# Performance work log

Measured on AMD Instinct MI355X. Metric: run time of the kernel, lower is better.

## Reference

```python
import jax, jax.numpy as jnp
import numpy as np

B, T, C = 4, 4096, 1024


def setup_inputs() -> dict:
    key = jax.random.key(0)
    ks = jax.random.split(key, 5)
    s = 1.0 / np.sqrt(C)
    x = jax.random.normal(ks[0], (B, T, C), dtype=jnp.float32)
    Wq = jax.random.normal(ks[1], (C, C), dtype=jnp.float32) * s
    Wk = jax.random.normal(ks[2], (C, C), dtype=jnp.float32) * s
    Wv = jax.random.normal(ks[3], (C, C), dtype=jnp.float32) * s
    Wo = jax.random.normal(ks[4], (C, C), dtype=jnp.float32) * s
    bo = jnp.zeros((C,), dtype=jnp.float32)
    return {"x": x, "Wq": Wq, "Wk": Wk, "Wv": Wv, "Wo": Wo, "bo": bo}


def reference(x, Wq, Wk, Wv, Wo, bo):
    # Single-head SDPA with causal additive mask; scale = 1/sqrt(C)
    q = jnp.einsum('btc,dc->btd', x, Wq)
    k = jnp.einsum('btc,dc->btd', x, Wk)
    v = jnp.einsum('btc,dc->btd', x, Wv)
    scale = 1.0 / jnp.sqrt(jnp.asarray(C, dtype=x.dtype))
    scores = jnp.einsum('btd,bsd->bts', q, k) * scale  # (B, T, T)
    t = scores.shape[1]
    causal = jnp.tril(jnp.ones((t, t), dtype=bool))
    scores = jnp.where(causal[None, :, :], scores, jnp.asarray(-jnp.inf, dtype=scores.dtype))
    attn = jax.nn.softmax(scores, axis=-1)
    out = jnp.einsum('bts,bsd->btd', attn, v)
    return jnp.einsum('btd,ed->bte', out, Wo) + bo
```

## Files before the change

### kernel.cpp

```cpp
#include <hip/hip_runtime.h>

typedef __bf16 bf16;
typedef __bf16 bf16x4 __attribute__((ext_vector_type(4)));
typedef __bf16 bf16x8 __attribute__((ext_vector_type(8)));
typedef float  f32x4  __attribute__((ext_vector_type(4)));

#define BM 128
#define BN 128
#define BK 64

__device__ __forceinline__ void async_copy16(const void* g, void* l) {
    __builtin_amdgcn_global_load_lds(
        (__attribute__((address_space(1))) void*)(g),
        (__attribute__((address_space(3))) void*)(l),
        16, 0, 0);
}

__global__ __launch_bounds__(256)
void gemm_nt(const bf16* __restrict__ A, int lda, size_t az,
             const bf16* __restrict__ B, int ldb, size_t bz,
             void* __restrict__ C0, void* __restrict__ C1, void* __restrict__ C2,
             int ldc, size_t cz,
             int M, int N, int K, float alpha,
             const float* __restrict__ bias,
             const float* __restrict__ row_scale, int rsz,
             int out_bf16, int qkv_mode, int causal_skip, int kcap,
             int row_off, int rev_m)
{
    int z  = blockIdx.z;
    int by = rev_m ? (gridDim.y - 1 - blockIdx.y) : blockIdx.y;
    int m0 = by * BM;
    int n0 = blockIdx.x * BN;
    if (causal_skip && n0 > row_off + m0 + BM - 1) return;
    int Keff = kcap ? min(K, row_off + m0 + BM) : K;
    A += (size_t)z * az;
    B += (size_t)z * bz;

    __shared__ __attribute__((aligned(16))) bf16 As[BM * BK];
    __shared__ __attribute__((aligned(16))) bf16 Bs[BN * BK];

    int tid  = threadIdx.x;
    int lane = tid & 63;
    int q    = lane >> 4;
    int r    = lane & 15;
    int wave = tid >> 6;
    int wm   = (wave >> 1) * 64;
    int wn   = (wave & 1) * 64;
    int sw   = r & 7;
    int gsw  = (((tid & 7) ^ ((tid >> 3) & 7)) * 8);

    f32x4 acc[4][4];
#pragma unroll
    for (int i = 0; i < 4; i++)
#pragma unroll
        for (int j = 0; j < 4; j++) acc[i][j] = (f32x4){0.f, 0.f, 0.f, 0.f};

    const bf16* Ag = A + (size_t)(m0 + (tid >> 3)) * lda + gsw;
    const bf16* Bg = B + (size_t)(n0 + (tid >> 3)) * ldb + gsw;
    char* lAs = (char*)As + tid * 16;
    char* lBs = (char*)Bs + tid * 16;
    size_t astep = (size_t)32 * lda;
    size_t bstep = (size_t)32 * ldb;

    for (int k0 = 0; k0 < Keff; k0 += BK) {
#pragma unroll
        for (int i = 0; i < 4; i++) {
            async_copy16(Ag + k0 + i * astep, lAs + i * 4096);
            async_copy16(Bg + k0 + i * bstep, lBs + i * 4096);
        }
        asm volatile("s_waitcnt vmcnt(0)" ::: "memory");
        __syncthreads();

#pragma unroll
        for (int kk = 0; kk < 2; kk++) {
            bf16x8 av[4], bv[4];
#pragma unroll
            for (int mi = 0; mi < 4; mi++)
                av[mi] = *(const bf16x8*)&As[(wm + mi * 16 + r) * BK
                                            + (((kk << 2) + q) ^ sw) * 8];
#pragma unroll
            for (int ni = 0; ni < 4; ni++)
                bv[ni] = *(const bf16x8*)&Bs[(wn + ni * 16 + r) * BK
                                            + (((kk << 2) + q) ^ sw) * 8];
#pragma unroll
            for (int mi = 0; mi < 4; mi++)
#pragma unroll
                for (int ni = 0; ni < 4; ni++)
                    acc[mi][ni] = __builtin_amdgcn_mfma_f32_16x16x32_bf16(
                        av[mi], bv[ni], acc[mi][ni], 0, 0, 0);
        }
        __syncthreads();
    }

    const float* rs = row_scale ? row_scale + (size_t)z * rsz : nullptr;
    void* Cb = C0;
    if (qkv_mode) { int sel = n0 >> 10; Cb = sel == 0 ? C0 : (sel == 1 ? C1 : C2); }
#pragma unroll
    for (int mi = 0; mi < 4; mi++) {
#pragma unroll
        for (int ni = 0; ni < 4; ni++) {
#pragma unroll
            for (int j = 0; j < 4; j++) {
                int row = m0 + wm + mi * 16 + q * 4 + j;
                int col = n0 + wn + ni * 16 + r;
                if (qkv_mode) col &= 1023;
                float v = acc[mi][ni][j] * alpha;
                if (rs)   v *= rs[row];
                if (bias) v += bias[col];
                if (out_bf16) ((bf16*)Cb + (size_t)z * cz)[(size_t)row * ldc + col] = (bf16)v;
                else          ((float*)Cb + (size_t)z * cz)[(size_t)row * ldc + col] = v;
            }
        }
    }
}

__global__ __launch_bounds__(256)
void softmax_causal(bf16* __restrict__ S, float* __restrict__ inv_l,
                    int T, int toff, int chunk)
{
    int tr = blockIdx.x, z = blockIdx.y;
    int t  = toff + tr;
    int L  = t + 1;
    int Lw = ((t >> 7) + 1) << 7;
    bf16* row = S + ((size_t)z * chunk + tr) * T;
    int tid = threadIdx.x;
    __shared__ float buf[4096];
    __shared__ float red[4];

    for (int s = tid * 8; s < Lw; s += 2048) {
        bf16x8 v = *(const bf16x8*)(row + s);
#pragma unroll
        for (int i = 0; i < 8; i++)
            buf[s + i] = (s + i < L) ? (float)v[i] : -3.0e38f;
    }
    __syncthreads();

    float m = -3.0e38f;
    for (int s = tid; s < Lw; s += 256) m = fmaxf(m, buf[s]);
#pragma unroll
    for (int off = 32; off > 0; off >>= 1) m = fmaxf(m, __shfl_down(m, off, 64));
    if ((tid & 63) == 0) red[tid >> 6] = m;
    __syncthreads();
    m = fmaxf(fmaxf(red[0], red[1]), fmaxf(red[2], red[3]));
    __syncthreads();

    float sum = 0.f;
    for (int s = tid * 8; s < Lw; s += 2048) {
        bf16x8 o;
#pragma unroll
        for (int i = 0; i < 8; i++) {
            float e = __expf(buf[s + i] - m);
            sum += e;
            o[i] = (bf16)e;
        }
        *(bf16x8*)(row + s) = o;
    }
#pragma unroll
    for (int off = 32; off > 0; off >>= 1) sum += __shfl_down(sum, off, 64);
    if ((tid & 63) == 0) red[tid >> 6] = sum;
    __syncthreads();
    if (tid == 0) inv_l[(size_t)z * chunk + tr] = 1.0f / (red[0] + red[1] + red[2] + red[3]);
}

__global__ __launch_bounds__(256)
void transpose64(const bf16* __restrict__ V, bf16* __restrict__ VT, int T, int C)
{
    __shared__ bf16 tile[64][65];
    int b  = blockIdx.z;
    int s0 = blockIdx.x * 64, d0 = blockIdx.y * 64;
    const bf16* Vb  = V  + (size_t)b * T * C;
    bf16*       VTb = VT + (size_t)b * T * C;
    int tx = threadIdx.x & 63, ty = threadIdx.x >> 6;
#pragma unroll
    for (int i = 0; i < 64; i += 4)
        tile[ty + i][tx] = Vb[(size_t)(s0 + ty + i) * C + d0 + tx];
    __syncthreads();
#pragma unroll
    for (int i = 0; i < 64; i += 4)
        VTb[(size_t)(d0 + ty + i) * T + s0 + tx] = tile[tx][ty + i];
}

__global__ void cvt_f32_bf16(const float4* __restrict__ in, bf16x4* __restrict__ out, int n4)
{
    int i = blockIdx.x * blockDim.x + threadIdx.x;
    int stride = gridDim.x * blockDim.x;
    for (; i < n4; i += stride) {
        float4 v = in[i];
        bf16x4 o = { (bf16)v.x, (bf16)v.y, (bf16)v.z, (bf16)v.w };
        out[i] = o;
    }
}

extern "C" void kernel_launch(void* const* d_in, const int* in_sizes, int n_in,
                              void* d_out, int out_size, void* d_ws, size_t ws_size,
                              hipStream_t stream)
{
    const int B = 4, T = 4096, C = 1024, M = B * T;
    const float* x  = (const float*)d_in[0];
    const float* Wq = (const float*)d_in[1];
    const float* Wk = (const float*)d_in[2];
    const float* Wv = (const float*)d_in[3];
    const float* Wo = (const float*)d_in[4];
    const float* bo = (const float*)d_in[5];
    float* out = (float*)d_out;

    char* ws = (char*)d_ws;
    size_t off = 0;
    auto alloc = [&](size_t bytes) -> char* {
        char* p = ws + off;
        off += (bytes + 255) & ~(size_t)255;
        return p;
    };
    bf16* Wcat = (bf16*)alloc((size_t)3 * C * C * 2);
    bf16* Wob  = (bf16*)alloc((size_t)C * C * 2);
    bf16* Qb   = (bf16*)alloc((size_t)M * C * 2);
    bf16* Kb   = (bf16*)alloc((size_t)M * C * 2);
    bf16* VT   = (bf16*)alloc((size_t)M * C * 2);

    size_t base = off;
    int chunk = T;
    bf16 *S, *xb, *Vtmp, *Ob;
    float* inv_l;
    {
        size_t need = base + (((size_t)B * T * T * 2 + 255) & ~(size_t)255)
                           + (((size_t)B * T * 4 + 255) & ~(size_t)255);
        if (need <= ws_size) {
            S     = (bf16*)alloc((size_t)B * T * T * 2);
            inv_l = (float*)alloc((size_t)B * T * 4);
            xb    = S;
            Vtmp  = S + (size_t)M * C;
            Ob    = Qb;
        } else {
            Ob = (bf16*)alloc((size_t)M * C * 2);
            chunk = T / 2;
            while (chunk > 1024) {
                size_t nd = off + (((size_t)B * chunk * T * 2 + 255) & ~(size_t)255)
                                + (((size_t)B * chunk * 4 + 255) & ~(size_t)255);
                if (nd <= ws_size) break;
                chunk >>= 1;
            }
            S     = (bf16*)alloc((size_t)B * chunk * T * 2);
            inv_l = (float*)alloc((size_t)B * chunk * 4);
            xb    = S;
            Vtmp  = Ob;
        }
    }

    dim3 blk(256);

    cvt_f32_bf16<<<dim3(4096), blk, 0, stream>>>((const float4*)x,  (bf16x4*)xb, M * C / 4);
    cvt_f32_bf16<<<dim3(1024), blk, 0, stream>>>((const float4*)Wq, (bf16x4*)(Wcat),             C * C / 4);
    cvt_f32_bf16<<<dim3(1024), blk, 0, stream>>>((const float4*)Wk, (bf16x4*)(Wcat + C * C),     C * C / 4);
    cvt_f32_bf16<<<dim3(1024), blk, 0, stream>>>((const float4*)Wv, (bf16x4*)(Wcat + 2 * C * C), C * C / 4);
    cvt_f32_bf16<<<dim3(1024), blk, 0, stream>>>((const float4*)Wo, (bf16x4*)Wob, C * C / 4);

    gemm_nt<<<dim3(3 * C / BN, M / BM, 1), blk, 0, stream>>>(
        xb, C, 0, Wcat, C, 0, Qb, Kb, Vtmp, C, 0, M, 3 * C, C, 1.f,
        nullptr, nullptr, 0, 1, 1, 0, 0, 0, 0);
    transpose64<<<dim3(T / 64, C / 64, B), blk, 0, stream>>>(Vtmp, VT, T, C);

    const float scale = 0.03125f;
    for (int toff = 0; toff < T; toff += chunk) {
        gemm_nt<<<dim3(T / BN, chunk / BM, B), blk, 0, stream>>>(
            Qb + (size_t)toff * C, C, (size_t)T * C,
            Kb, C, (size_t)T * C,
            S, nullptr, nullptr, T, (size_t)chunk * T,
            chunk, T, C, scale,
            nullptr, nullptr, 0, 1, 0, 1, 0, toff, 1);
        softmax_causal<<<dim3(chunk, B), blk, 0, stream>>>(S, inv_l, T, toff, chunk);
        gemm_nt<<<dim3(C / BN, chunk / BM, B), blk, 0, stream>>>(
            S, T, (size_t)chunk * T,
            VT, T, (size_t)T * C,
            Ob + (size_t)toff * C, nullptr, nullptr, C, (size_t)T * C,
            chunk, C, T, 1.f,
            nullptr, inv_l, chunk, 1, 0, 0, 1, toff, 1);
    }

    gemm_nt<<<dim3(C / BN, M / BM, 1), blk, 0, stream>>>(
        Ob, C, 0, Wob, C, 0, out, nullptr, nullptr, C, 0, M, C, C, 1.f,
        bo, nullptr, 0, 0, 0, 0, 0, 0, 0);
}
```

Baseline: 672.1 us.

## Enlarge GEMM tiles to 256x256 with double-buffered, phase-interleaved LDS pipeline

The GEMM kernel moves to 256x256 tiles with 512 threads (8 waves), a double-buffered LDS ring, and a four-phase loop. Each phase issues the next tile's async global-to-LDS loads, reads LDS fragments and runs MFMAs under raised wave priority, with explicit barriers and waitcnts. The goal is to hide global load latency behind compute and raise arithmetic intensity per block. The softmax causal padding width changes to 256 to match the new tile. In exchange, LDS use and register pressure are much higher, and small grids (e.g. the output projection with 4x64 blocks) may leave CUs underutilized.

```diff
diff --git a/kernel.cpp b/kernel.cpp
--- a/kernel.cpp
+++ b/kernel.cpp
@@ -5,8 +5,8 @@
 typedef __bf16 bf16x8 __attribute__((ext_vector_type(8)));
 typedef float  f32x4  __attribute__((ext_vector_type(4)));
 
-#define BM 128
-#define BN 128
+#define BM 256
+#define BN 256
 #define BK 64
 
 __device__ __forceinline__ void async_copy16(const void* g, void* l) {
@@ -16,7 +16,36 @@
         16, 0, 0);
 }
 
-__global__ __launch_bounds__(256)
+#define RD_A(mi, kk) (*(const bf16x8*)&As[par][(wm + (mi)*16 + r) * BK + ((((kk)<<2) + q) ^ sw) * 8])
+#define RD_B(ni, kk) (*(const bf16x8*)&Bs[par][(wn + (ni)*16 + r) * BK + ((((kk)<<2) + q) ^ sw) * 8])
+
+#define MM(p) do { \
+    __builtin_amdgcn_s_setprio(1); \
+    _Pragma("unroll") \
+    for (int jj = 0; jj < 2; jj++) { \
+        _Pragma("unroll") \
+        for (int ni = 0; ni < 4; ni++) { \
+            _Pragma("unroll") \
+            for (int kk = 0; kk < 2; kk++) \
+                acc[2*(p)+jj][ni] = __builtin_amdgcn_mfma_f32_16x16x32_bf16( \
+                    av[jj][kk], bv[ni][kk], acc[2*(p)+jj][ni], 0, 0, 0); \
+        } \
+    } \
+    __builtin_amdgcn_s_setprio(0); \
+} while (0)
+
+#define PHASE_TAIL(p) do { \
+    __builtin_amdgcn_sched_barrier(0); \
+    __builtin_amdgcn_s_barrier(); \
+    asm volatile("s_waitcnt lgkmcnt(0)" ::: "memory"); \
+    __builtin_amdgcn_sched_barrier(0); \
+    MM(p); \
+    __builtin_amdgcn_sched_barrier(0); \
+    __builtin_amdgcn_s_barrier(); \
+    __builtin_amdgcn_sched_barrier(0); \
+} while (0)
+
+__global__ __launch_bounds__(512, 2)
 void gemm_nt(const bf16* __restrict__ A, int lda, size_t az,
              const bf16* __restrict__ B, int ldb, size_t bz,
              void* __restrict__ C0, void* __restrict__ C1, void* __restrict__ C2,
@@ -33,70 +62,98 @@
     int n0 = blockIdx.x * BN;
     if (causal_skip && n0 > row_off + m0 + BM - 1) return;
     int Keff = kcap ? min(K, row_off + m0 + BM) : K;
+    int nk = Keff / BK;
     A += (size_t)z * az;
     B += (size_t)z * bz;
 
-    __shared__ __attribute__((aligned(16))) bf16 As[BM * BK];
-    __shared__ __attribute__((aligned(16))) bf16 Bs[BN * BK];
+    __shared__ __attribute__((aligned(16))) bf16 As[2][BM * BK];
+    __shared__ __attribute__((aligned(16))) bf16 Bs[2][BN * BK];
 
     int tid  = threadIdx.x;
     int lane = tid & 63;
     int q    = lane >> 4;
     int r    = lane & 15;
     int wave = tid >> 6;
-    int wm   = (wave >> 1) * 64;
-    int wn   = (wave & 1) * 64;
+    int wm   = (wave >> 2) * 128;
+    int wn   = (wave & 3) * 64;
     int sw   = r & 7;
     int gsw  = (((tid & 7) ^ ((tid >> 3) & 7)) * 8);
 
-    f32x4 acc[4][4];
-#pragma unroll
-    for (int i = 0; i < 4; i++)
+    f32x4 acc[8][4];
+#pragma unroll
+    for (int i = 0; i < 8; i++)
 #pragma unroll
         for (int j = 0; j < 4; j++) acc[i][j] = (f32x4){0.f, 0.f, 0.f, 0.f};
 
     const bf16* Ag = A + (size_t)(m0 + (tid >> 3)) * lda + gsw;
     const bf16* Bg = B + (size_t)(n0 + (tid >> 3)) * ldb + gsw;
-    char* lAs = (char*)As + tid * 16;
-    char* lBs = (char*)Bs + tid * 16;
-    size_t astep = (size_t)32 * lda;
-    size_t bstep = (size_t)32 * ldb;
-
-    for (int k0 = 0; k0 < Keff; k0 += BK) {
-#pragma unroll
-        for (int i = 0; i < 4; i++) {
-            async_copy16(Ag + k0 + i * astep, lAs + i * 4096);
-            async_copy16(Bg + k0 + i * bstep, lBs + i * 4096);
+    char* lA = (char*)&As[0][0] + tid * 16;
+    char* lB = (char*)&Bs[0][0] + tid * 16;
+    size_t a64 = (size_t)64 * lda;
+    size_t b64 = (size_t)64 * ldb;
+
+    auto stA = [&](int kt, int h, int pb) {
+        const bf16* g = Ag + (size_t)kt * BK + (h ? 2 * a64 : 0);
+        char* l = lA + pb * 32768 + h * 16384;
+        async_copy16(g, l);
+        async_copy16(g + a64, l + 8192);
+    };
+    auto stB = [&](int kt, int h, int pb) {
+        const bf16* g = Bg + (size_t)kt * BK + (h ? 2 * b64 : 0);
+        char* l = lB + pb * 32768 + h * 16384;
+        async_copy16(g, l);
+        async_copy16(g + b64, l + 8192);
+    };
+
+    stA(0, 0, 0); stA(0, 1, 0);
+    stB(0, 0, 0); stB(0, 1, 0);
+    if (nk > 1) {
+        stB(1, 0, 1); stB(1, 1, 1);
+        asm volatile("s_waitcnt vmcnt(4)" ::: "memory");
+    } else {
+        asm volatile("s_waitcnt vmcnt(0)" ::: "memory");
+    }
+    __builtin_amdgcn_sched_barrier(0);
+    __builtin_amdgcn_s_barrier();
+    __builtin_amdgcn_sched_barrier(0);
+
+    for (int t = 0; t < nk; ++t) {
+        int par = t & 1;
+        bf16x8 av[2][2], bv[4][2];
+
+        if (t + 1 < nk) stA(t + 1, 0, par ^ 1);
+#pragma unroll
+        for (int ni = 0; ni < 4; ni++) { bv[ni][0] = RD_B(ni, 0); bv[ni][1] = RD_B(ni, 1); }
+        av[0][0] = RD_A(0, 0); av[0][1] = RD_A(0, 1);
+        av[1][0] = RD_A(1, 0); av[1][1] = RD_A(1, 1);
+        asm volatile("s_waitcnt lgkmcnt(8)" ::: "memory");
+        PHASE_TAIL(0);
+
+        if (t + 1 < nk) stA(t + 1, 1, par ^ 1);
+        av[0][0] = RD_A(2, 0); av[0][1] = RD_A(2, 1);
+        av[1][0] = RD_A(3, 0); av[1][1] = RD_A(3, 1);
+        PHASE_TAIL(1);
+
+        if (t + 2 < nk) stB(t + 2, 0, par);
+        av[0][0] = RD_A(4, 0); av[0][1] = RD_A(4, 1);
+        av[1][0] = RD_A(5, 0); av[1][1] = RD_A(5, 1);
+        PHASE_TAIL(2);
+
+        if (t + 2 < nk) stB(t + 2, 1, par);
+        av[0][0] = RD_A(6, 0); av[0][1] = RD_A(6, 1);
+        av[1][0] = RD_A(7, 0); av[1][1] = RD_A(7, 1);
+        if (t + 1 < nk) {
+            if (t + 2 < nk) asm volatile("s_waitcnt vmcnt(4)" ::: "memory");
+            else            asm volatile("s_waitcnt vmcnt(0)" ::: "memory");
         }
-        asm volatile("s_waitcnt vmcnt(0)" ::: "memory");
-        __syncthreads();
-
-#pragma unroll
-        for (int kk = 0; kk < 2; kk++) {
-            bf16x8 av[4], bv[4];
-#pragma unroll
-            for (int mi = 0; mi < 4; mi++)
-                av[mi] = *(const bf16x8*)&As[(wm + mi * 16 + r) * BK
-                                            + (((kk << 2) + q) ^ sw) * 8];
-#pragma unroll
-            for (int ni = 0; ni < 4; ni++)
-                bv[ni] = *(const bf16x8*)&Bs[(wn + ni * 16 + r) * BK
-                                            + (((kk << 2) + q) ^ sw) * 8];
-#pragma unroll
-            for (int mi = 0; mi < 4; mi++)
-#pragma unroll
-                for (int ni = 0; ni < 4; ni++)
-                    acc[mi][ni] = __builtin_amdgcn_mfma_f32_16x16x32_bf16(
-                        av[mi], bv[ni], acc[mi][ni], 0, 0, 0);
-        }
-        __syncthreads();
+        PHASE_TAIL(3);
     }
 
     const float* rs = row_scale ? row_scale + (size_t)z * rsz : nullptr;
     void* Cb = C0;
     if (qkv_mode) { int sel = n0 >> 10; Cb = sel == 0 ? C0 : (sel == 1 ? C1 : C2); }
 #pragma unroll
-    for (int mi = 0; mi < 4; mi++) {
+    for (int mi = 0; mi < 8; mi++) {
 #pragma unroll
         for (int ni = 0; ni < 4; ni++) {
 #pragma unroll
@@ -121,7 +178,7 @@
     int tr = blockIdx.x, z = blockIdx.y;
     int t  = toff + tr;
     int L  = t + 1;
-    int Lw = ((t >> 7) + 1) << 7;
+    int Lw = ((t >> 8) + 1) << 8;
     bf16* row = S + ((size_t)z * chunk + tr) * T;
     int tid = threadIdx.x;
     __shared__ float buf[4096];
@@ -247,6 +304,7 @@
     }
 
     dim3 blk(256);
+    dim3 gblk(512);
 
     cvt_f32_bf16<<<dim3(4096), blk, 0, stream>>>((const float4*)x,  (bf16x4*)xb, M * C / 4);
     cvt_f32_bf16<<<dim3(1024), blk, 0, stream>>>((const float4*)Wq, (bf16x4*)(Wcat),             C * C / 4);
@@ -254,21 +312,21 @@
     cvt_f32_bf16<<<dim3(1024), blk, 0, stream>>>((const float4*)Wv, (bf16x4*)(Wcat + 2 * C * C), C * C / 4);
     cvt_f32_bf16<<<dim3(1024), blk, 0, stream>>>((const float4*)Wo, (bf16x4*)Wob, C * C / 4);
 
-    gemm_nt<<<dim3(3 * C / BN, M / BM, 1), blk, 0, stream>>>(
+    gemm_nt<<<dim3(3 * C / BN, M / BM, 1), gblk, 0, stream>>>(
         xb, C, 0, Wcat, C, 0, Qb, Kb, Vtmp, C, 0, M, 3 * C, C, 1.f,
         nullptr, nullptr, 0, 1, 1, 0, 0, 0, 0);
     transpose64<<<dim3(T / 64, C / 64, B), blk, 0, stream>>>(Vtmp, VT, T, C);
 
     const float scale = 0.03125f;
     for (int toff = 0; toff < T; toff += chunk) {
-        gemm_nt<<<dim3(T / BN, chunk / BM, B), blk, 0, stream>>>(
+        gemm_nt<<<dim3(T / BN, chunk / BM, B), gblk, 0, stream>>>(
             Qb + (size_t)toff * C, C, (size_t)T * C,
             Kb, C, (size_t)T * C,
             S, nullptr, nullptr, T, (size_t)chunk * T,
             chunk, T, C, scale,
             nullptr, nullptr, 0, 1, 0, 1, 0, toff, 1);
         softmax_causal<<<dim3(chunk, B), blk, 0, stream>>>(S, inv_l, T, toff, chunk);
-        gemm_nt<<<dim3(C / BN, chunk / BM, B), blk, 0, stream>>>(
+        gemm_nt<<<dim3(C / BN, chunk / BM, B), gblk, 0, stream>>>(
             S, T, (size_t)chunk * T,
             VT, T, (size_t)T * C,
             Ob + (size_t)toff * C, nullptr, nullptr, C, (size_t)T * C,
@@ -276,7 +334,7 @@
             nullptr, inv_l, chunk, 1, 0, 0, 1, toff, 1);
     }
 
-    gemm_nt<<<dim3(C / BN, M / BM, 1), blk, 0, stream>>>(
+    gemm_nt<<<dim3(C / BN, M / BM, 1), gblk, 0, stream>>>(
         Ob, C, 0, Wob, C, 0, out, nullptr, nullptr, C, 0, M, C, C, 1.f,
         bo, nullptr, 0, 0, 0, 0, 0, 0, 0);
 }
```

Result: slower. 718.4 us (+6.9%).
